# Performance work log

Hardware: AMD Instinct MI355X
Metric: run time of the kernel (lower is better)

## Reference

```python
import jax, jax.numpy as jnp
import numpy as np

N, E, IN, HID, OUT = 50000, 800000, 64, 128, 2


def setup_inputs() -> dict:
    key = jax.random.key(0)
    ks = jax.random.split(key, 8)
    x = jax.random.normal(ks[0], (N, IN), dtype=jnp.float32)
    edge_index = jax.random.randint(ks[1], (2, E), 0, N, dtype=jnp.int32)
    def w(k, o, i):
        return jax.random.normal(k, (o, i), dtype=jnp.float32) * (1.0 / np.sqrt(i))
    return {
        "x": x,
        "edge_index": edge_index,
        "W_l0": w(ks[2], HID, IN),  "b_l0": jnp.zeros((HID,), jnp.float32), "W_r0": w(ks[3], HID, IN),
        "W_l1": w(ks[4], HID, HID), "b_l1": jnp.zeros((HID,), jnp.float32), "W_r1": w(ks[5], HID, HID),
        "W_fc": w(ks[6], OUT, HID), "b_fc": jnp.zeros((OUT,), jnp.float32),
    }


def _sage_conv(x, src, dst, deg_inv, W_l, b_l, W_r):
    # mean-aggregate neighbor features: gather x[src], scatter-add into dst, divide by degree
    agg = jax.ops.segment_sum(x[src], dst, num_segments=x.shape[0]) * deg_inv[:, None]
    # PyG SAGEConv: lin_l(aggregated) + lin_r(root); bias lives in lin_l
    return agg @ W_l.T + b_l + x @ W_r.T


def reference(x, edge_index, W_l0, b_l0, W_r0, W_l1, b_l1, W_r1, W_fc, b_fc):
    src, dst = edge_index[0], edge_index[1]
    deg = jax.ops.segment_sum(jnp.ones((E,), jnp.float32), dst, num_segments=N)
    deg_inv = 1.0 / jnp.maximum(deg, 1.0)
    h = jax.nn.relu(_sage_conv(x, src, dst, deg_inv, W_l0, b_l0, W_r0))
    # dropout is identity in eval mode (training=False)
    h = jax.nn.relu(_sage_conv(h, src, dst, deg_inv, W_l1, b_l1, W_r1))
    return h @ W_fc.T + b_fc
```

## Files before the change

kernel.cpp:

```cpp
#include <hip/hip_runtime.h>
#include <hip/hip_bf16.h>

#define NN   50000
#define NE   800000
#define NBK  625
#define NH   196

typedef __attribute__((ext_vector_type(8))) short short8;
typedef __attribute__((ext_vector_type(4))) float f32x4;
typedef __attribute__((ext_vector_type(2))) float f32x2;

static __device__ __forceinline__ ushort f2bf(float f) {
    union { float f; unsigned u; } v; v.f = f;
    unsigned r = v.u + 0x7fffu + ((v.u >> 16) & 1u);
    return (ushort)(r >> 16);
}
static __device__ __forceinline__ float bf2f(ushort h) {
    union { unsigned u; float f; } v; v.u = ((unsigned)h) << 16;
    return v.f;
}

static __device__ __forceinline__ int exscan256(int* s, int tid, int v) {
    __syncthreads();
    s[tid] = v;
    __syncthreads();
    #pragma unroll
    for (int off = 1; off < 256; off <<= 1) {
        int a = (tid >= off) ? s[tid - off] : 0;
        __syncthreads();
        s[tid] += a;
        __syncthreads();
    }
    return s[tid] - v;
}

__global__ __launch_bounds__(256) void hist1_k(
    const int* __restrict__ dst, int* __restrict__ ghist,
    const float* __restrict__ x, ushort* __restrict__ xb,
    unsigned* __restrict__ x8w,
    const float* __restrict__ Wl0, const float* __restrict__ Wr0,
    const float* __restrict__ Wl1, const float* __restrict__ Wr1,
    ushort* __restrict__ wbt0, ushort* __restrict__ wbt1)
{
    __shared__ int hist[256];
    int tid = threadIdx.x, b = blockIdx.x;
    int gid = b * 256 + tid;
    hist[tid] = 0;

    if (gid < 2048) {
        {
            int c = gid;
            int n  = c >> 4;
            int kc = (c & 15) * 8;
            const float* wsrc = (kc < 64) ? (Wl0 + n * 64 + kc) : (Wr0 + n * 64 + (kc - 64));
            float4 f0 = *(const float4*)(wsrc);
            float4 f1 = *(const float4*)(wsrc + 4);
            short8 v;
            v[0] = f2bf(f0.x); v[1] = f2bf(f0.y); v[2] = f2bf(f0.z); v[3] = f2bf(f0.w);
            v[4] = f2bf(f1.x); v[5] = f2bf(f1.y); v[6] = f2bf(f1.z); v[7] = f2bf(f1.w);
            int byte = (n * 256 + kc * 2) ^ ((n & 7) << 4);
            *(short8*)((char*)wbt0 + byte) = v;
        }
        #pragma unroll
        for (int rep = 0; rep < 2; ++rep) {
            int c = gid + rep * 2048;
            int n  = c >> 5;
            int kc = (c & 31) * 8;
            int h  = (kc >= 128);
            int kk = kc - h * 128;
            const float* wsrc = h ? (Wr1 + n * 128 + kk) : (Wl1 + n * 128 + kk);
            float4 f0 = *(const float4*)(wsrc);
            float4 f1 = *(const float4*)(wsrc + 4);
            short8 v;
            v[0] = f2bf(f0.x); v[1] = f2bf(f0.y); v[2] = f2bf(f0.z); v[3] = f2bf(f0.w);
            v[4] = f2bf(f1.x); v[5] = f2bf(f1.y); v[6] = f2bf(f1.z); v[7] = f2bf(f1.w);
            int byte = h * 32768 + ((n * 256 + kk * 2) ^ ((n & 7) << 4));
            *(short8*)((char*)wbt1 + byte) = v;
        }
    }

    #pragma unroll
    for (int k5 = 0; k5 < 5; ++k5) {
        int idx = k5 * 160000 + gid;
        float4 f = ((const float4*)x)[idx];
        ushort4 o;
        o.x = f2bf(f.x); o.y = f2bf(f.y); o.z = f2bf(f.z); o.w = f2bf(f.w);
        ((ushort4*)xb)[idx] = o;
        unsigned q = 0;
        q = __builtin_amdgcn_cvt_pk_fp8_f32(f.x, f.y, q, false);
        q = __builtin_amdgcn_cvt_pk_fp8_f32(f.z, f.w, q, true);
        x8w[idx] = q;
    }

    __syncthreads();
    int eb = b * 1280;
    #pragma unroll
    for (int j = 0; j < 5; ++j) {
        int e = eb + j * 256 + tid;
        atomicAdd(&hist[dst[e] >> 8], 1);
    }
    __syncthreads();
    ghist[b * 256 + tid] = hist[tid];
}

__global__ __launch_bounds__(256) void scan1_k(
    const int* __restrict__ ghist, int* __restrict__ gbase,
    int* __restrict__ dtot)
{
    __shared__ int s[256];
    int tid = threadIdx.x, h = blockIdx.x;
    int carry = 0;
    for (int c = 0; c < 3; ++c) {
        int idx = c * 256 + tid;
        int v = (idx < NBK) ? ghist[idx * 256 + h] : 0;
        int ex = exscan256(s, tid, v);
        if (idx < NBK) gbase[idx * 256 + h] = carry + ex;
        carry += s[255];
        __syncthreads();
    }
    if (tid == 0) dtot[h] = carry;
}

__global__ __launch_bounds__(256) void scat1_k(
    const int* __restrict__ src, const int* __restrict__ dst,
    const int* __restrict__ gbase, const int* __restrict__ dtot,
    unsigned* __restrict__ buf1)
{
    __shared__ int sc[256], hist[256], lbase[256], cur[256], dbase[256], gb[256];
    __shared__ unsigned sorted[1280];
    int tid = threadIdx.x, b = blockIdx.x;
    hist[tid] = 0;
    gb[tid] = gbase[b * 256 + tid];
    int dv = (tid < NH) ? dtot[tid] : 0;
    int eb = b * 1280;
    unsigned k[5]; int dg[5];
    __syncthreads();
    #pragma unroll
    for (int j = 0; j < 5; ++j) {
        int e = eb + j * 256 + tid;
        int d_ = dst[e];
        k[j]  = ((unsigned)d_ << 16) | (unsigned)src[e];
        dg[j] = d_ >> 8;
        atomicAdd(&hist[dg[j]], 1);
    }
    __syncthreads();
    int ex = exscan256(sc, tid, hist[tid]);
    lbase[tid] = ex; cur[tid] = ex;
    int dbx = exscan256(sc, tid, dv);
    dbase[tid] = dbx;
    __syncthreads();
    #pragma unroll
    for (int j = 0; j < 5; ++j) {
        int lr = atomicAdd(&cur[dg[j]], 1);
        sorted[lr] = k[j];
    }
    __syncthreads();
    #pragma unroll
    for (int j = 0; j < 5; ++j) {
        int i = j * 256 + tid;
        unsigned kk = sorted[i];
        int dig = (int)(kk >> 24);
        int pos = dbase[dig] + gb[dig] + (i - lbase[dig]);
        buf1[pos] = kk;
    }
}

__global__ __launch_bounds__(256) void build_k(
    const unsigned* __restrict__ buf1, const int* __restrict__ dtot,
    int* __restrict__ rowptr, ushort* __restrict__ nbr16)
{
    __shared__ int sc[256], degs[256], lb[256], cur[256];
    __shared__ ushort sorted[6400];
    int tid = threadIdx.x, h = blockIdx.x;
    int dv = (tid < NH) ? dtot[tid] : 0;
    (void)exscan256(sc, tid, dv);
    int start = (h == 0) ? 0 : sc[h - 1];
    int end   = sc[h];
    degs[tid] = 0;
    __syncthreads();
    for (int e = start + tid; e < end; e += 256)
        atomicAdd(&degs[(buf1[e] >> 16) & 255], 1);
    __syncthreads();
    int lbv = exscan256(sc, tid, degs[tid]);
    lb[tid] = lbv; cur[tid] = lbv;
    int n = h * 256 + tid;
    if (n <= NN) rowptr[n] = start + lbv;
    __syncthreads();
    for (int e = start + tid; e < end; e += 256) {
        unsigned kk = buf1[e];
        int d = (int)((kk >> 16) & 255u);
        int lr = atomicAdd(&cur[d], 1);
        sorted[lr] = (ushort)(kk & 0xffffu);
    }
    __syncthreads();
    int sz = end - start;
    for (int i = tid; i < sz; i += 256)
        nbr16[start + i] = sorted[i];
}

__global__ __launch_bounds__(256) void gather0_k(
    const unsigned char* __restrict__ x8, const int* __restrict__ rowptr,
    const ushort* __restrict__ nbr, ushort* __restrict__ agg0)
{
    int node = (blockIdx.x * 256 + threadIdx.x) >> 3;
    int sub  = threadIdx.x & 7;
    if (node >= NN) return;
    int b = rowptr[node], e2 = rowptr[node + 1];
    float acc[8];
    #pragma unroll
    for (int j = 0; j < 8; ++j) acc[j] = 0.f;

    int e = b;
    for (; e + 4 <= e2; e += 4) {
        int s0 = nbr[e], s1 = nbr[e + 1], s2 = nbr[e + 2], s3 = nbr[e + 3];
        uint2 w0 = *(const uint2*)(x8 + s0 * 64 + sub * 8);
        uint2 w1 = *(const uint2*)(x8 + s1 * 64 + sub * 8);
        uint2 w2 = *(const uint2*)(x8 + s2 * 64 + sub * 8);
        uint2 w3 = *(const uint2*)(x8 + s3 * 64 + sub * 8);
        #pragma unroll
        for (int q = 0; q < 4; ++q) {
            uint2 w = (q == 0) ? w0 : (q == 1) ? w1 : (q == 2) ? w2 : w3;
            f32x2 f01 = __builtin_amdgcn_cvt_pk_f32_fp8(w.x, false);
            f32x2 f23 = __builtin_amdgcn_cvt_pk_f32_fp8(w.x, true);
            f32x2 f45 = __builtin_amdgcn_cvt_pk_f32_fp8(w.y, false);
            f32x2 f67 = __builtin_amdgcn_cvt_pk_f32_fp8(w.y, true);
            acc[0] += f01[0]; acc[1] += f01[1];
            acc[2] += f23[0]; acc[3] += f23[1];
            acc[4] += f45[0]; acc[5] += f45[1];
            acc[6] += f67[0]; acc[7] += f67[1];
        }
    }
    for (; e < e2; ++e) {
        int s = nbr[e];
        uint2 w = *(const uint2*)(x8 + s * 64 + sub * 8);
        f32x2 f01 = __builtin_amdgcn_cvt_pk_f32_fp8(w.x, false);
        f32x2 f23 = __builtin_amdgcn_cvt_pk_f32_fp8(w.x, true);
        f32x2 f45 = __builtin_amdgcn_cvt_pk_f32_fp8(w.y, false);
        f32x2 f67 = __builtin_amdgcn_cvt_pk_f32_fp8(w.y, true);
        acc[0] += f01[0]; acc[1] += f01[1];
        acc[2] += f23[0]; acc[3] += f23[1];
        acc[4] += f45[0]; acc[5] += f45[1];
        acc[6] += f67[0]; acc[7] += f67[1];
    }

    float inv = 1.0f / fmaxf((float)(e2 - b), 1.0f);
    short8 o;
    #pragma unroll
    for (int j = 0; j < 8; ++j) o[j] = (short)f2bf(acc[j] * inv);
    *(short8*)(agg0 + node * 64 + sub * 8) = o;
}

__global__ __launch_bounds__(256) void gather1_k(
    const unsigned char* __restrict__ h8, const int* __restrict__ rowptr,
    const ushort* __restrict__ nbr, ushort* __restrict__ agg1)
{
    int node = (blockIdx.x * 256 + threadIdx.x) >> 4;
    int sub  = threadIdx.x & 15;
    if (node >= NN) return;
    int b = rowptr[node], e2 = rowptr[node + 1];
    float acc[8];
    #pragma unroll
    for (int j = 0; j < 8; ++j) acc[j] = 0.f;

    int e = b;
    for (; e + 4 <= e2; e += 4) {
        int s0 = nbr[e], s1 = nbr[e + 1], s2 = nbr[e + 2], s3 = nbr[e + 3];
        uint2 w0 = *(const uint2*)(h8 + s0 * 128 + sub * 8);
        uint2 w1 = *(const uint2*)(h8 + s1 * 128 + sub * 8);
        uint2 w2 = *(const uint2*)(h8 + s2 * 128 + sub * 8);
        uint2 w3 = *(const uint2*)(h8 + s3 * 128 + sub * 8);
        #pragma unroll
        for (int q = 0; q < 4; ++q) {
            uint2 w = (q == 0) ? w0 : (q == 1) ? w1 : (q == 2) ? w2 : w3;
            f32x2 f01 = __builtin_amdgcn_cvt_pk_f32_fp8(w.x, false);
            f32x2 f23 = __builtin_amdgcn_cvt_pk_f32_fp8(w.x, true);
            f32x2 f45 = __builtin_amdgcn_cvt_pk_f32_fp8(w.y, false);
            f32x2 f67 = __builtin_amdgcn_cvt_pk_f32_fp8(w.y, true);
            acc[0] += f01[0]; acc[1] += f01[1];
            acc[2] += f23[0]; acc[3] += f23[1];
            acc[4] += f45[0]; acc[5] += f45[1];
            acc[6] += f67[0]; acc[7] += f67[1];
        }
    }
    for (; e < e2; ++e) {
        int s = nbr[e];
        uint2 w = *(const uint2*)(h8 + s * 128 + sub * 8);
        f32x2 f01 = __builtin_amdgcn_cvt_pk_f32_fp8(w.x, false);
        f32x2 f23 = __builtin_amdgcn_cvt_pk_f32_fp8(w.x, true);
        f32x2 f45 = __builtin_amdgcn_cvt_pk_f32_fp8(w.y, false);
        f32x2 f67 = __builtin_amdgcn_cvt_pk_f32_fp8(w.y, true);
        acc[0] += f01[0]; acc[1] += f01[1];
        acc[2] += f23[0]; acc[3] += f23[1];
        acc[4] += f45[0]; acc[5] += f45[1];
        acc[6] += f67[0]; acc[7] += f67[1];
    }

    float inv = 1.0f / fmaxf((float)(e2 - b), 1.0f);
    #pragma unroll
    for (int j = 0; j < 8; ++j)
        agg1[node * 128 + j * 16 + sub] = f2bf(acc[j] * inv);
}

__global__ __launch_bounds__(256) void dense0_k(
    const ushort* __restrict__ xb, const ushort* __restrict__ agg0,
    const ushort* __restrict__ wbt0, const float* __restrict__ bl,
    ushort* __restrict__ h0, unsigned char* __restrict__ h8)
{
    __shared__ ushort bt[128 * 128];
    __shared__ float  bl_s[128];

    #pragma unroll
    for (int c = 0; c < 8; ++c) {
        int i = threadIdx.x + c * 256;
        ((short8*)bt)[i] = ((const short8*)wbt0)[i];
    }
    if (threadIdx.x < 128) bl_s[threadIdx.x] = bl[threadIdx.x];
    __syncthreads();

    int w = threadIdx.x >> 6, l = threadIdx.x & 63;
    int l15 = l & 15, hi = l >> 4;
    int row  = blockIdx.x * 64 + w * 16 + l15;
    int rowc = row < NN ? row : 0;

    short8 a[4];
    a[0] = *(const short8*)(agg0 + rowc * 64 + hi * 8);
    a[1] = *(const short8*)(agg0 + rowc * 64 + 32 + hi * 8);
    a[2] = *(const short8*)(xb + rowc * 64 + hi * 8);
    a[3] = *(const short8*)(xb + rowc * 64 + 32 + hi * 8);

    f32x4 acc[8];
    #pragma unroll
    for (int nt = 0; nt < 8; ++nt) acc[nt] = (f32x4){0.f, 0.f, 0.f, 0.f};

    #pragma unroll
    for (int ks = 0; ks < 4; ++ks) {
        #pragma unroll
        for (int nt = 0; nt < 8; ++nt) {
            int byte = ((nt * 16 + l15) * 256 + (ks * 32 + hi * 8) * 2) ^ ((l15 & 7) << 4);
            short8 bfr = *(const short8*)((const char*)bt + byte);
            acc[nt] = __builtin_amdgcn_mfma_f32_16x16x32_bf16(a[ks], bfr, acc[nt], 0, 0, 0);
        }
    }

    int rowbase = blockIdx.x * 64 + w * 16 + hi * 4;
    #pragma unroll
    for (int r = 0; r < 4; ++r) {
        int ro = rowbase + r;
        if (ro < NN) {
            float v[8];
            #pragma unroll
            for (int nt = 0; nt < 8; ++nt) {
                int col = nt * 16 + l15;
                v[nt] = fmaxf(acc[nt][r] + bl_s[col], 0.f);
                h0[ro * 128 + col] = f2bf(v[nt]);
            }
            unsigned lo = 0, hiw = 0;
            lo  = __builtin_amdgcn_cvt_pk_fp8_f32(v[0], v[1], lo, false);
            lo  = __builtin_amdgcn_cvt_pk_fp8_f32(v[2], v[3], lo, true);
            hiw = __builtin_amdgcn_cvt_pk_fp8_f32(v[4], v[5], hiw, false);
            hiw = __builtin_amdgcn_cvt_pk_fp8_f32(v[6], v[7], hiw, true);
            uint2 q; q.x = lo; q.y = hiw;
            *(uint2*)(h8 + ro * 128 + l15 * 8) = q;
        }
    }
}

__global__ __launch_bounds__(256) void dense1_k(
    const ushort* __restrict__ h0, const ushort* __restrict__ agg1,
    const ushort* __restrict__ wbt1, const float* __restrict__ bl,
    const float* __restrict__ Wfc, const float* __restrict__ bfc,
    float* __restrict__ out)
{
    __shared__ ushort bt[128 * 128];
    __shared__ float  bl_s[128];
    __shared__ float  wfc_s[256];

    #pragma unroll
    for (int c = 0; c < 8; ++c) {
        int i = threadIdx.x + c * 256;
        ((short8*)bt)[i] = ((const short8*)wbt1)[i];
    }
    if (threadIdx.x < 128) bl_s[threadIdx.x] = bl[threadIdx.x];
    if (threadIdx.x < 256) wfc_s[threadIdx.x] = Wfc[threadIdx.x];
    __syncthreads();

    int w = threadIdx.x >> 6, l = threadIdx.x & 63;
    int l15 = l & 15, hi = l >> 4;
    int row  = blockIdx.x * 64 + w * 16 + l15;
    int rowc = row < NN ? row : 0;

    short8 a[8];
    #pragma unroll
    for (int ks = 0; ks < 4; ++ks)
        a[ks] = *(const short8*)(agg1 + rowc * 128 + ks * 32 + hi * 8);
    #pragma unroll
    for (int ks = 0; ks < 4; ++ks)
        a[4 + ks] = *(const short8*)(h0 + rowc * 128 + ks * 32 + hi * 8);

    f32x4 acc[8];
    #pragma unroll
    for (int nt = 0; nt < 8; ++nt) acc[nt] = (f32x4){0.f, 0.f, 0.f, 0.f};

    #pragma unroll
    for (int ks = 0; ks < 4; ++ks) {
        #pragma unroll
        for (int nt = 0; nt < 8; ++nt) {
            int byte = ((nt * 16 + l15) * 256 + (ks * 32 + hi * 8) * 2) ^ ((l15 & 7) << 4);
            short8 bfr = *(const short8*)((const char*)bt + byte);
            acc[nt] = __builtin_amdgcn_mfma_f32_16x16x32_bf16(a[ks], bfr, acc[nt], 0, 0, 0);
        }
    }
    __syncthreads();
    #pragma unroll
    for (int c = 0; c < 8; ++c) {
        int i = threadIdx.x + c * 256;
        ((short8*)bt)[i] = ((const short8*)(wbt1 + 16384))[i];
    }
    __syncthreads();
    #pragma unroll
    for (int ks = 0; ks < 4; ++ks) {
        #pragma unroll
        for (int nt = 0; nt < 8; ++nt) {
            int byte = ((nt * 16 + l15) * 256 + (ks * 32 + hi * 8) * 2) ^ ((l15 & 7) << 4);
            short8 bfr = *(const short8*)((const char*)bt + byte);
            acc[nt] = __builtin_amdgcn_mfma_f32_16x16x32_bf16(a[4 + ks], bfr, acc[nt], 0, 0, 0);
        }
    }

    int rowbase = blockIdx.x * 64 + w * 16 + hi * 4;
    #pragma unroll
    for (int r = 0; r < 4; ++r) {
        float p0 = 0.f, p1 = 0.f;
        #pragma unroll
        for (int nt = 0; nt < 8; ++nt) {
            int col = nt * 16 + l15;
            float h1 = fmaxf(acc[nt][r] + bl_s[col], 0.f);
            p0 += h1 * wfc_s[col];
            p1 += h1 * wfc_s[128 + col];
        }
        p0 += __shfl_xor(p0, 1, 64); p0 += __shfl_xor(p0, 2, 64);
        p0 += __shfl_xor(p0, 4, 64); p0 += __shfl_xor(p0, 8, 64);
        p1 += __shfl_xor(p1, 1, 64); p1 += __shfl_xor(p1, 2, 64);
        p1 += __shfl_xor(p1, 4, 64); p1 += __shfl_xor(p1, 8, 64);
        int ro = rowbase + r;
        if (l15 == 0 && ro < NN) {
            float2 o; o.x = p0 + bfc[0]; o.y = p1 + bfc[1];
            *(float2*)(out + ro * 2) = o;
        }
    }
}

extern "C" void kernel_launch(void* const* d_in, const int* in_sizes, int n_in,
                              void* d_out, int out_size, void* d_ws, size_t ws_size,
                              hipStream_t stream)
{
    const float* x   = (const float*)d_in[0];
    const int*   ei  = (const int*)d_in[1];
    const float* Wl0 = (const float*)d_in[2];
    const float* bl0 = (const float*)d_in[3];
    const float* Wr0 = (const float*)d_in[4];
    const float* Wl1 = (const float*)d_in[5];
    const float* bl1 = (const float*)d_in[6];
    const float* Wr1 = (const float*)d_in[7];
    const float* Wfc = (const float*)d_in[8];
    const float* bfc = (const float*)d_in[9];
    float* out = (float*)d_out;

    const int* src = ei;
    const int* dst = ei + NE;

    char*     ws     = (char*)d_ws;
    unsigned* buf1   = (unsigned*)(ws);
    ushort*   nbr16  = (ushort*)(ws + 3200000);
    int*      rowptr = (int*)(ws + 4800000);
    int*      ghist  = (int*)(ws + 5000016);
    int*      gbase  = (int*)(ws + 5640016);
    int*      dtot   = (int*)(ws + 6280016);
    ushort*   aggB   = (ushort*)(ws + 6281056);
    ushort*   h0B    = (ushort*)(ws + 19081056);
    ushort*   xb     = (ushort*)(ws + 31881056);
    unsigned* x8w    = (unsigned*)(ws + 38281056);
    ushort*   wbt0   = (ushort*)(ws + 41481056);
    ushort*   wbt1   = (ushort*)(ws + 41513824);
    unsigned char* h8 = (unsigned char*)(ws + 41579360);

    hist1_k<<<NBK, 256, 0, stream>>>(dst, ghist, x, xb, x8w,
                                     Wl0, Wr0, Wl1, Wr1, wbt0, wbt1);
    scan1_k<<<NH, 256, 0, stream>>>(ghist, gbase, dtot);
    scat1_k<<<NBK, 256, 0, stream>>>(src, dst, gbase, dtot, buf1);
    build_k<<<NH, 256, 0, stream>>>(buf1, dtot, rowptr, nbr16);

    gather0_k<<<1563, 256, 0, stream>>>((const unsigned char*)x8w, rowptr, nbr16, aggB);
    dense0_k <<<782, 256, 0, stream>>>(xb, aggB, wbt0, bl0, h0B, h8);
    gather1_k<<<3125, 256, 0, stream>>>(h8, rowptr, nbr16, aggB);
    dense1_k <<<782, 256, 0, stream>>>(h0B, aggB, wbt1, bl1, Wfc, bfc, out);
}
```

Before: 91.89 us.

## Use 200 edge blocks and move x/weight conversion into scan kernel

Edge partitioning for the counting sort drops from 625 blocks of 1280 edges to 200 blocks of 4000 edges. The bucket scan therefore becomes a single 256-wide exclusive scan instead of three chunked passes. The x-to-bf16/fp8 conversion and the weight packing move from the histogram kernel into the scan kernel, which was otherwise nearly idle with 196 blocks. The histogram kernel becomes a pure histogram. The trade-off is fewer blocks in the histogram and scatter kernels, so occupancy drops, and the scatter kernel needs more shared memory and registers per block.

```diff
diff --git a/kernel.cpp b/kernel.cpp
--- a/kernel.cpp
+++ b/kernel.cpp
@@ -3,7 +3,8 @@
 
 #define NN   50000
 #define NE   800000
-#define NBK  625
+#define NBK  200
+#define EPB  4000
 #define NH   196
 
 typedef __attribute__((ext_vector_type(8))) short short8;
@@ -35,17 +36,34 @@
 }
 
 __global__ __launch_bounds__(256) void hist1_k(
-    const int* __restrict__ dst, int* __restrict__ ghist,
+    const int* __restrict__ dst, int* __restrict__ ghist)
+{
+    __shared__ int hist[256];
+    int tid = threadIdx.x, b = blockIdx.x;
+    hist[tid] = 0;
+    __syncthreads();
+    int eb = b * EPB;
+    #pragma unroll
+    for (int j = 0; j < 16; ++j) {
+        int o = j * 256 + tid;
+        if (o < EPB) atomicAdd(&hist[dst[eb + o] >> 8], 1);
+    }
+    __syncthreads();
+    ghist[b * 256 + tid] = hist[tid];
+}
+
+__global__ __launch_bounds__(256) void scan1_k(
+    const int* __restrict__ ghist, int* __restrict__ gbase,
+    int* __restrict__ dtot,
     const float* __restrict__ x, ushort* __restrict__ xb,
     unsigned* __restrict__ x8w,
     const float* __restrict__ Wl0, const float* __restrict__ Wr0,
     const float* __restrict__ Wl1, const float* __restrict__ Wr1,
     ushort* __restrict__ wbt0, ushort* __restrict__ wbt1)
 {
-    __shared__ int hist[256];
-    int tid = threadIdx.x, b = blockIdx.x;
-    int gid = b * 256 + tid;
-    hist[tid] = 0;
+    __shared__ int s[256];
+    int tid = threadIdx.x, h = blockIdx.x;
+    int gid = h * 256 + tid;
 
     if (gid < 2048) {
         {
@@ -66,59 +84,38 @@
             int c = gid + rep * 2048;
             int n  = c >> 5;
             int kc = (c & 31) * 8;
-            int h  = (kc >= 128);
-            int kk = kc - h * 128;
-            const float* wsrc = h ? (Wr1 + n * 128 + kk) : (Wl1 + n * 128 + kk);
+            int hh = (kc >= 128);
+            int kk = kc - hh * 128;
+            const float* wsrc = hh ? (Wr1 + n * 128 + kk) : (Wl1 + n * 128 + kk);
             float4 f0 = *(const float4*)(wsrc);
             float4 f1 = *(const float4*)(wsrc + 4);
             short8 v;
             v[0] = f2bf(f0.x); v[1] = f2bf(f0.y); v[2] = f2bf(f0.z); v[3] = f2bf(f0.w);
             v[4] = f2bf(f1.x); v[5] = f2bf(f1.y); v[6] = f2bf(f1.z); v[7] = f2bf(f1.w);
-            int byte = h * 32768 + ((n * 256 + kk * 2) ^ ((n & 7) << 4));
+            int byte = hh * 32768 + ((n * 256 + kk * 2) ^ ((n & 7) << 4));
             *(short8*)((char*)wbt1 + byte) = v;
         }
     }
 
-    #pragma unroll
-    for (int k5 = 0; k5 < 5; ++k5) {
-        int idx = k5 * 160000 + gid;
-        float4 f = ((const float4*)x)[idx];
-        ushort4 o;
-        o.x = f2bf(f.x); o.y = f2bf(f.y); o.z = f2bf(f.z); o.w = f2bf(f.w);
-        ((ushort4*)xb)[idx] = o;
-        unsigned q = 0;
-        q = __builtin_amdgcn_cvt_pk_fp8_f32(f.x, f.y, q, false);
-        q = __builtin_amdgcn_cvt_pk_fp8_f32(f.z, f.w, q, true);
-        x8w[idx] = q;
-    }
-
-    __syncthreads();
-    int eb = b * 1280;
-    #pragma unroll
-    for (int j = 0; j < 5; ++j) {
-        int e = eb + j * 256 + tid;
-        atomicAdd(&hist[dst[e] >> 8], 1);
-    }
-    __syncthreads();
-    ghist[b * 256 + tid] = hist[tid];
-}
-
-__global__ __launch_bounds__(256) void scan1_k(
-    const int* __restrict__ ghist, int* __restrict__ gbase,
-    int* __restrict__ dtot)
-{
-    __shared__ int s[256];
-    int tid = threadIdx.x, h = blockIdx.x;
-    int carry = 0;
-    for (int c = 0; c < 3; ++c) {
-        int idx = c * 256 + tid;
-        int v = (idx < NBK) ? ghist[idx * 256 + h] : 0;
-        int ex = exscan256(s, tid, v);
-        if (idx < NBK) gbase[idx * 256 + h] = carry + ex;
-        carry += s[255];
-        __syncthreads();
-    }
-    if (tid == 0) dtot[h] = carry;
+    int v = (tid < NBK) ? ghist[tid * 256 + h] : 0;
+    int ex = exscan256(s, tid, v);
+    if (tid < NBK) gbase[tid * 256 + h] = ex;
+    if (tid == 0) dtot[h] = s[255];
+
+    #pragma unroll
+    for (int r = 0; r < 16; ++r) {
+        int idx = r * 50176 + gid;
+        if (idx < 800000) {
+            float4 f = ((const float4*)x)[idx];
+            ushort4 o;
+            o.x = f2bf(f.x); o.y = f2bf(f.y); o.z = f2bf(f.z); o.w = f2bf(f.w);
+            ((ushort4*)xb)[idx] = o;
+            unsigned q = 0;
+            q = __builtin_amdgcn_cvt_pk_fp8_f32(f.x, f.y, q, false);
+            q = __builtin_amdgcn_cvt_pk_fp8_f32(f.z, f.w, q, true);
+            x8w[idx] = q;
+        }
+    }
 }
 
 __global__ __launch_bounds__(256) void scat1_k(
@@ -127,21 +124,25 @@
     unsigned* __restrict__ buf1)
 {
     __shared__ int sc[256], hist[256], lbase[256], cur[256], dbase[256], gb[256];
-    __shared__ unsigned sorted[1280];
+    __shared__ unsigned sorted[EPB];
     int tid = threadIdx.x, b = blockIdx.x;
     hist[tid] = 0;
     gb[tid] = gbase[b * 256 + tid];
     int dv = (tid < NH) ? dtot[tid] : 0;
-    int eb = b * 1280;
-    unsigned k[5]; int dg[5];
-    __syncthreads();
-    #pragma unroll
-    for (int j = 0; j < 5; ++j) {
-        int e = eb + j * 256 + tid;
-        int d_ = dst[e];
-        k[j]  = ((unsigned)d_ << 16) | (unsigned)src[e];
-        dg[j] = d_ >> 8;
-        atomicAdd(&hist[dg[j]], 1);
+    int eb = b * EPB;
+    unsigned k[16]; int dg[16];
+    __syncthreads();
+    #pragma unroll
+    for (int j = 0; j < 16; ++j) {
+        int o = j * 256 + tid;
+        dg[j] = -1;
+        if (o < EPB) {
+            int e = eb + o;
+            int d_ = dst[e];
+            k[j]  = ((unsigned)d_ << 16) | (unsigned)src[e];
+            dg[j] = d_ >> 8;
+            atomicAdd(&hist[dg[j]], 1);
+        }
     }
     __syncthreads();
     int ex = exscan256(sc, tid, hist[tid]);
@@ -150,18 +151,22 @@
     dbase[tid] = dbx;
     __syncthreads();
     #pragma unroll
-    for (int j = 0; j < 5; ++j) {
-        int lr = atomicAdd(&cur[dg[j]], 1);
-        sorted[lr] = k[j];
-    }
-    __syncthreads();
-    #pragma unroll
-    for (int j = 0; j < 5; ++j) {
+    for (int j = 0; j < 16; ++j) {
+        if (dg[j] >= 0) {
+            int lr = atomicAdd(&cur[dg[j]], 1);
+            sorted[lr] = k[j];
+        }
+    }
+    __syncthreads();
+    #pragma unroll
+    for (int j = 0; j < 16; ++j) {
         int i = j * 256 + tid;
-        unsigned kk = sorted[i];
-        int dig = (int)(kk >> 24);
-        int pos = dbase[dig] + gb[dig] + (i - lbase[dig]);
-        buf1[pos] = kk;
+        if (i < EPB) {
+            unsigned kk = sorted[i];
+            int dig = (int)(kk >> 24);
+            int pos = dbase[dig] + gb[dig] + (i - lbase[dig]);
+            buf1[pos] = kk;
+        }
     }
 }
 
@@ -474,19 +479,19 @@
     ushort*   nbr16  = (ushort*)(ws + 3200000);
     int*      rowptr = (int*)(ws + 4800000);
     int*      ghist  = (int*)(ws + 5000016);
-    int*      gbase  = (int*)(ws + 5640016);
-    int*      dtot   = (int*)(ws + 6280016);
-    ushort*   aggB   = (ushort*)(ws + 6281056);
-    ushort*   h0B    = (ushort*)(ws + 19081056);
-    ushort*   xb     = (ushort*)(ws + 31881056);
-    unsigned* x8w    = (unsigned*)(ws + 38281056);
-    ushort*   wbt0   = (ushort*)(ws + 41481056);
-    ushort*   wbt1   = (ushort*)(ws + 41513824);
-    unsigned char* h8 = (unsigned char*)(ws + 41579360);
-
-    hist1_k<<<NBK, 256, 0, stream>>>(dst, ghist, x, xb, x8w,
-                                     Wl0, Wr0, Wl1, Wr1, wbt0, wbt1);
-    scan1_k<<<NH, 256, 0, stream>>>(ghist, gbase, dtot);
+    int*      gbase  = (int*)(ws + 5204816);
+    int*      dtot   = (int*)(ws + 5409616);
+    ushort*   aggB   = (ushort*)(ws + 5410656);
+    ushort*   h0B    = (ushort*)(ws + 18210656);
+    ushort*   xb     = (ushort*)(ws + 31010656);
+    unsigned* x8w    = (unsigned*)(ws + 37410656);
+    ushort*   wbt0   = (ushort*)(ws + 40610656);
+    ushort*   wbt1   = (ushort*)(ws + 40643424);
+    unsigned char* h8 = (unsigned char*)(ws + 40708960);
+
+    hist1_k<<<NBK, 256, 0, stream>>>(dst, ghist);
+    scan1_k<<<NH, 256, 0, stream>>>(ghist, gbase, dtot, x, xb, x8w,
+                                    Wl0, Wr0, Wl1, Wr1, wbt0, wbt1);
     scat1_k<<<NBK, 256, 0, stream>>>(src, dst, gbase, dtot, buf1);
     build_k<<<NH, 256, 0, stream>>>(buf1, dtot, rowptr, nbr16);
 
```

Result: slower. 96.23 us (+4.7%).
